# Kernel tuning notes

Measured on AMD Instinct MI355X. Metric: run time of the kernel, lower is better.

Reference implementation:

```python
import jax, jax.numpy as jnp
import numpy as np

EPS = 1e-8

def _cosine_rows(a, b):
    na = jnp.maximum(jnp.linalg.norm(a, axis=1), EPS)
    nb = jnp.maximum(jnp.linalg.norm(b, axis=1), EPS)
    return jnp.sum(a * b, axis=1) / (na * nb)


def setup_inputs() -> dict:
    key = jax.random.key(0)
    k1, k2 = jax.random.split(key)
    X = jax.random.normal(k1, (16384, 1024), dtype=jnp.float32)
    dictionary = jax.random.normal(k2, (4096, 1024), dtype=jnp.float32)
    descriptors = jnp.arange(4096, dtype=jnp.int64)
    return {"X": X, "dictionary": dictionary, "descriptors": descriptors, "k": 16}


def reference(X, dictionary, descriptors, k):
    # SOMP with centering=True, criterion='l1', pc=None (default forward path)
    orig_X = X
    std_orig_sum = jnp.sum(jnp.var(orig_X, axis=0, ddof=1))
    X_mean = jnp.mean(X, axis=0, keepdims=True)   # [1, D]
    Xc = X - X_mean                               # centered data [N, D]

    M = dictionary.shape[0]
    notchosen = jnp.ones((M,), dtype=X.dtype)
    residual = Xc
    chosen, evr, l2, cosine = [], [], [], []
    W = None
    recon = jnp.zeros_like(Xc)

    for i in range(k):  # k is a static Python int -> unrolled, per-step shapes static
        cross = residual @ dictionary.T           # [N, M] -- dominant memory traffic
        scores = jnp.sum(jnp.abs(cross * notchosen), axis=0)  # l1 criterion
        idx = jnp.argmax(scores)
        chosen.append(idx)
        notchosen = notchosen.at[idx].set(0)

        atoms = dictionary[jnp.stack(chosen)]     # [i+1, D], dynamic gather, static shape
        # least squares: min ||atoms.T @ W - Xc.T||  (full column rank -> normal eqs)
        G = atoms @ atoms.T                       # [i+1, i+1]
        W = jnp.linalg.solve(G, atoms @ Xc.T)     # [i+1, N]
        recon = (atoms.T @ W).T                   # [N, D]
        residual = Xc - recon

        rec_full = X_mean + recon
        evr.append(jnp.sum(jnp.var(rec_full, axis=0, ddof=1)) / std_orig_sum)
        cosine.append(jnp.mean(_cosine_rows(orig_X, rec_full)))
        l2.append(jnp.mean((orig_X - rec_full) ** 2))

    weights = jnp.linalg.norm(W, axis=1)          # [k]
    chosen_arr = jnp.stack(chosen)
    recon_out = X_mean + recon
    residual_out = Xc - recon                     # == X - recon_out
    return (recon_out, residual_out, chosen_arr, weights, W.T,
            jnp.stack(evr), jnp.stack(l2), jnp.stack(cosine))
```

## Files before the change

### kernel.cpp

```cpp
#include <hip/hip_runtime.h>
#include <math.h>

#define NROWS 16384
#define DIMK  1024
#define MDIC  4096
#define KSEL  16

#define OFF_RECON   0
#define OFF_RESID   ((size_t)NROWS*DIMK)
#define OFF_CHOSEN  ((size_t)2*NROWS*DIMK)
#define OFF_WEIGHTS (OFF_CHOSEN + 16)
#define OFF_WT      (OFF_WEIGHTS + 16)
#define OFF_EVR     (OFF_WT + (size_t)NROWS*KSEL)
#define OFF_L2      (OFF_EVR + 16)
#define OFF_COS     (OFF_L2 + 16)

typedef unsigned short u16;
typedef unsigned long long u64;
typedef __attribute__((ext_vector_type(8))) short short8;
typedef __attribute__((ext_vector_type(4))) float f32x4;

__device__ inline float blockReduce256f(float v) {
    __shared__ float ws_[4];
    #pragma unroll
    for (int off = 32; off > 0; off >>= 1) v += __shfl_down(v, off);
    __syncthreads();
    if ((threadIdx.x & 63) == 0) ws_[threadIdx.x >> 6] = v;
    __syncthreads();
    return ws_[0] + ws_[1] + ws_[2] + ws_[3];
}

__device__ inline void wredStore(double v, int k, int lane, int wv, double (*accS)[4]) {
    #pragma unroll
    for (int off = 32; off > 0; off >>= 1) v += __shfl_down(v, off);
    if (lane == 0) accS[k][wv] = v;
}

__device__ inline u16 f2bf(float f) {
    unsigned u = __float_as_uint(f);
    unsigned r = u + 0x7FFFu + ((u >> 16) & 1u);
    return (u16)(r >> 16);
}
__device__ inline float bf2f(u16 h) { return __uint_as_float(((unsigned)h) << 16); }

__global__ void k_init(float* notchosen, u64* amx, u64* statsAcc, u64* ctr2) {
    int m = blockIdx.x * 256 + threadIdx.x;
    if (m < MDIC) notchosen[m] = 1.0f;
    if (blockIdx.x == 0) {
        if (threadIdx.x < 40) statsAcc[threadIdx.x] = 0ULL;
        if (threadIdx.x < 2)  amx[threadIdx.x] = 0ULL;
        if (threadIdx.x == 0) *ctr2 = 0ULL;
    }
}

__global__ __launch_bounds__(256) void k_colstats(const float* __restrict__ X,
                                                  float* __restrict__ colpart,
                                                  float* __restrict__ sqpart) {
    int d  = blockIdx.x * 256 + threadIdx.x;
    int r0 = blockIdx.y * 256;
    float s = 0.f, sq = 0.f;
    for (int r = 0; r < 256; ++r) {
        float v = X[(size_t)(r0 + r) * DIMK + d];
        s += v; sq += v * v;
    }
    colpart[(size_t)blockIdx.y * DIMK + d] = s;
    __shared__ float red[256];
    red[threadIdx.x] = sq; __syncthreads();
    for (int off = 128; off > 0; off >>= 1) {
        if (threadIdx.x < off) red[threadIdx.x] += red[threadIdx.x + off];
        __syncthreads();
    }
    if (threadIdx.x == 0) sqpart[blockIdx.y * 4 + blockIdx.x] = red[0];
}

__global__ __launch_bounds__(1024) void k_reduce_mean(const float* __restrict__ colpart,
                                                      const float* __restrict__ sqpart,
                                                      float* __restrict__ xmean,
                                                      double* __restrict__ scal) {
    int d = threadIdx.x;
    double s = 0.0;
    for (int y = 0; y < 64; ++y) s += (double)colpart[(size_t)y * DIMK + d];
    float m = (float)(s / (double)NROWS);
    xmean[d] = m;
    __shared__ double red[1024];
    red[d] = (double)m * (double)m; __syncthreads();
    for (int off = 512; off > 0; off >>= 1) {
        if (d < off) red[d] += red[d + off];
        __syncthreads();
    }
    if (d == 0) {
        double xmn2 = red[0];
        double sx2 = 0.0;
        for (int i = 0; i < 256; ++i) sx2 += (double)sqpart[i];
        scal[0] = sx2;
        scal[1] = sx2 - (double)NROWS * xmn2;
        scal[2] = xmn2;
    }
}

__global__ __launch_bounds__(256) void k_md(const float* __restrict__ Dict,
                                            const float* __restrict__ xmean,
                                            float* __restrict__ md,
                                            float* __restrict__ Dnorm2) {
    int m = blockIdx.x, t = threadIdx.x;
    float4 a = ((const float4*)(Dict + (size_t)m * DIMK))[t];
    float4 b = ((const float4*)xmean)[t];
    float s  = a.x * b.x + a.y * b.y + a.z * b.z + a.w * b.w;
    float sn = a.x * a.x + a.y * a.y + a.z * a.z + a.w * a.w;
    s  = blockReduce256f(s);
    sn = blockReduce256f(sn);
    if (t == 0) { md[m] = s; Dnorm2[m] = sn; }
}

__global__ __launch_bounds__(256) void k_split(const float* __restrict__ src,
                                               u16* __restrict__ hi,
                                               u16* __restrict__ lo) {
    size_t idx = ((size_t)blockIdx.x * 256 + threadIdx.x) * 4;
    float4 v = *(const float4*)(src + idx);
    ushort4 h, l;
    h.x = f2bf(v.x); l.x = f2bf(v.x - bf2f(h.x));
    h.y = f2bf(v.y); l.y = f2bf(v.y - bf2f(h.y));
    h.z = f2bf(v.z); l.z = f2bf(v.z - bf2f(h.z));
    h.w = f2bf(v.w); l.w = f2bf(v.w - bf2f(h.w));
    *(ushort4*)(hi + idx) = h;
    *(ushort4*)(lo + idx) = l;
}

__global__ __launch_bounds__(256) void k_splitX(const float* __restrict__ src,
                                                u16* __restrict__ hi,
                                                u16* __restrict__ lo,
                                                const float* __restrict__ xmean,
                                                float* __restrict__ Xnorm2,
                                                float* __restrict__ XdotM) {
    int n = blockIdx.x, t = threadIdx.x;
    size_t idx = (size_t)n * DIMK + t * 4;
    float4 v = *(const float4*)(src + idx);
    float4 mv = ((const float4*)xmean)[t];
    ushort4 h, l;
    h.x = f2bf(v.x); l.x = f2bf(v.x - bf2f(h.x));
    h.y = f2bf(v.y); l.y = f2bf(v.y - bf2f(h.y));
    h.z = f2bf(v.z); l.z = f2bf(v.z - bf2f(h.z));
    h.w = f2bf(v.w); l.w = f2bf(v.w - bf2f(h.w));
    *(ushort4*)(hi + idx) = h;
    *(ushort4*)(lo + idx) = l;
    float s2 = v.x * v.x + v.y * v.y + v.z * v.z + v.w * v.w;
    float sm = v.x * mv.x + v.y * mv.y + v.z * mv.z + v.w * mv.w;
    s2 = blockReduce256f(s2);
    sm = blockReduce256f(sm);
    if (t == 0) { Xnorm2[n] = s2; XdotM[n] = sm; }
}

__global__ __launch_bounds__(256) void k_gemm_mfma(const u16* __restrict__ Ahi,
                                                   const u16* __restrict__ Alo,
                                                   const u16* __restrict__ Bhi,
                                                   const u16* __restrict__ Blo,
                                                   const float* __restrict__ md,
                                                   u16* __restrict__ C0h,
                                                   int rowAbase) {
    __shared__ u16 sAh[128 * 32];
    __shared__ u16 sAl[128 * 32];
    __shared__ u16 sBh[128 * 32];
    __shared__ u16 sBl[128 * 32];
    int tid  = threadIdx.x;
    int wave = tid >> 6, lane = tid & 63;
    int rowA0 = blockIdx.y * 128;
    int rowB0 = blockIdx.x * 128;

    const u16* gsrc = (wave == 0) ? Ahi : (wave == 1) ? Alo : (wave == 2) ? Bhi : Blo;
    u16* sdst       = (wave == 0) ? sAh : (wave == 1) ? sAl : (wave == 2) ? sBh : sBl;
    int grow0 = (wave < 2) ? rowA0 : rowB0;
    const u16* gbase = gsrc + (size_t)(grow0 + (lane >> 2)) * DIMK + ((lane & 3) << 3);

    f32x4 zero = {0.f, 0.f, 0.f, 0.f};
    f32x4 acc[4][4];
    #pragma unroll
    for (int i = 0; i < 4; ++i)
        #pragma unroll
        for (int j = 0; j < 4; ++j) acc[i][j] = zero;

    int lm = lane & 15, lk = lane >> 4;
    int wi = wave >> 1, wj = wave & 1;

    for (int k0 = 0; k0 < DIMK; k0 += 32) {
        __syncthreads();
        #pragma unroll
        for (int i = 0; i < 8; ++i) {
            __builtin_amdgcn_global_load_lds(
                (__attribute__((address_space(1))) void*)(gbase + k0 + (size_t)i * 16 * DIMK),
                (__attribute__((address_space(3))) void*)(sdst + i * 512),
                16, 0, 0);
        }
        __syncthreads();
        short8 ah[4], al[4], bh[4], bl[4];
        #pragma unroll
        for (int f = 0; f < 4; ++f) {
            int ra = (wi * 64 + f * 16 + lm) * 32 + lk * 8;
            ah[f] = *(const short8*)&sAh[ra];
            al[f] = *(const short8*)&sAl[ra];
            int rb = (wj * 64 + f * 16 + lm) * 32 + lk * 8;
            bh[f] = *(const short8*)&sBh[rb];
            bl[f] = *(const short8*)&sBl[rb];
        }
        #pragma unroll
        for (int fi = 0; fi < 4; ++fi)
            #pragma unroll
            for (int fj = 0; fj < 4; ++fj) {
                acc[fi][fj] = __builtin_amdgcn_mfma_f32_16x16x32_bf16(ah[fi], bh[fj], acc[fi][fj], 0, 0, 0);
                acc[fi][fj] = __builtin_amdgcn_mfma_f32_16x16x32_bf16(ah[fi], bl[fj], acc[fi][fj], 0, 0, 0);
                acc[fi][fj] = __builtin_amdgcn_mfma_f32_16x16x32_bf16(al[fi], bh[fj], acc[fi][fj], 0, 0, 0);
            }
    }
    #pragma unroll
    for (int fj = 0; fj < 4; ++fj) {
        int m = rowB0 + wj * 64 + fj * 16 + lm;
        float mdv = md[m];
        #pragma unroll
        for (int fi = 0; fi < 4; ++fi) {
            int nb = rowAbase + rowA0 + wi * 64 + fi * 16 + lk * 4;
            #pragma unroll
            for (int r = 0; r < 4; ++r)
                C0h[(size_t)(nb + r) * MDIC + m] = f2bf(acc[fi][fj][r] - mdv);
        }
    }
}

template <int NA>
__global__ __launch_bounds__(256) void k_score(const u16* __restrict__ C0h,
                                               const float* __restrict__ GR,
                                               const float* __restrict__ Wm,
                                               float* __restrict__ scorePf) {
    constexpr int NAX = NA ? NA : 1;
    __shared__ float Wl[NAX][64];
    int t = threadIdx.x;
    int m0 = blockIdx.x * 1024 + t * 4;
    int n0 = blockIdx.y * 64;
    float4 gr[NAX];
    #pragma unroll
    for (int j = 0; j < NA; ++j) gr[j] = *(const float4*)&GR[(size_t)j * MDIC + m0];
    for (int idx = t; idx < NA * 64; idx += 256) {
        int j = idx >> 6, nn = idx & 63;
        Wl[j][nn] = Wm[(size_t)j * NROWS + n0 + nn];
    }
    __syncthreads();
    float4 acc = {0.f, 0.f, 0.f, 0.f};
    for (int nn = 0; nn < 64; ++nn) {
        ushort4 ch = *(const ushort4*)&C0h[(size_t)(n0 + nn) * MDIC + m0];
        float4 c = {bf2f(ch.x), bf2f(ch.y), bf2f(ch.z), bf2f(ch.w)};
        float4 cr = {0.f, 0.f, 0.f, 0.f};
        #pragma unroll
        for (int j = 0; j < NA; ++j) {
            float wv = Wl[j][nn];
            cr.x += wv * gr[j].x; cr.y += wv * gr[j].y;
            cr.z += wv * gr[j].z; cr.w += wv * gr[j].w;
        }
        acc.x += fabsf(c.x - cr.x); acc.y += fabsf(c.y - cr.y);
        acc.z += fabsf(c.z - cr.z); acc.w += fabsf(c.w - cr.w);
    }
    *(float4*)&scorePf[(size_t)blockIdx.y * MDIC + m0] = acc;
}

__global__ __launch_bounds__(256) void k_scoreargmax(const float* __restrict__ scorePf,
                                                     float* __restrict__ notchosen,
                                                     u64* __restrict__ amx,
                                                     int* __restrict__ chosen,
                                                     float* __restrict__ outChosen,
                                                     const float* __restrict__ md,
                                                     const float* __restrict__ Dnorm2,
                                                     const float* __restrict__ GR,
                                                     float* __restrict__ Lmat,
                                                     float* __restrict__ Gcc,
                                                     float* __restrict__ mdot,
                                                     int iter) {
    int t = threadIdx.x;
    int m0 = blockIdx.x * 256;
    int tm = t & 63, yg = t >> 6;
    float sx = 0.f, sy = 0.f, sz = 0.f, sw = 0.f;
    #pragma unroll 4
    for (int y = yg; y < 256; y += 4) {
        float4 v = *(const float4*)&scorePf[(size_t)y * MDIC + m0 + (tm << 2)];
        sx += v.x; sy += v.y; sz += v.z; sw += v.w;
    }
    __shared__ float4 red4[4][64];
    float4 pv; pv.x = sx; pv.y = sy; pv.z = sz; pv.w = sw;
    red4[yg][tm] = pv;
    __syncthreads();
    u64 best = 0ULL;
    if (t < 64) {
        float4 a = red4[0][t], b = red4[1][t], cc = red4[2][t], d = red4[3][t];
        double sv[4] = {(double)a.x + b.x + cc.x + d.x,
                        (double)a.y + b.y + cc.y + d.y,
                        (double)a.z + b.z + cc.z + d.z,
                        (double)a.w + b.w + cc.w + d.w};
        int mb = m0 + (t << 2);
        #pragma unroll
        for (int j = 0; j < 4; ++j) {
            if (notchosen[mb + j] != 0.f) {
                u64 key = ((u64)__double_as_longlong(sv[j]) & ~0xFFFULL) | (u64)(4095 - (mb + j));
                if (key > best) best = key;
            }
        }
        #pragma unroll
        for (int off = 32; off > 0; off >>= 1) {
            u64 o = __shfl_down(best, off);
            if (o > best) best = o;
        }
    }
    __shared__ int slast, sc;
    if (t == 0) {
        atomicMax(&amx[0], best);
        __threadfence();
        u64 done = atomicAdd(&amx[1], 1ULL);
        slast = (done == 15ULL) ? 1 : 0;
        if (slast) {
            u64 k = atomicMax(&amx[0], 0ULL);
            int c = 4095 - (int)(k & 0xFFFULL);
            sc = c;
            chosen[iter] = c;
            notchosen[c] = 0.f;
            outChosen[iter] = (float)c;
            mdot[iter] = md[c];
            amx[0] = 0ULL; amx[1] = 0ULL;
        }
    }
    __syncthreads();
    if (!slast) return;
    int c = sc;
    __shared__ float Lsh[16][16];
    __shared__ float g[17];
    __shared__ float LrowS[16];
    Lsh[t >> 4][t & 15] = Lmat[t];
    if (t < iter)  g[t] = GR[(size_t)t * MDIC + c];
    if (t == iter) g[t] = Dnorm2[c];
    __syncthreads();
    if (t == 0) {
        for (int b = 0; b < iter; ++b) {
            float s = g[b];
            for (int x = 0; x < b; ++x) s -= LrowS[x] * Lsh[b][x];
            LrowS[b] = s / Lsh[b][b];
        }
        float s2 = g[iter];
        for (int x = 0; x < iter; ++x) s2 -= LrowS[x] * LrowS[x];
        LrowS[iter] = sqrtf(fmaxf(s2, 1e-20f));
        for (int b = 0; b <= iter; ++b) Lmat[iter * 16 + b] = LrowS[b];
        for (int b = iter + 1; b < 16; ++b) Lmat[iter * 16 + b] = 0.f;
        for (int b = 0; b < iter; ++b) { Gcc[iter * 16 + b] = g[b]; Gcc[b * 16 + iter] = g[b]; }
        Gcc[iter * 16 + iter] = g[iter];
    }
}

template <int NAT>
__global__ __launch_bounds__(256) void k_gramsolve(const float* __restrict__ Dict,
                                                   const int* __restrict__ chosen,
                                                   const u16* __restrict__ C0h,
                                                   float* __restrict__ GR,
                                                   float* __restrict__ Bm,
                                                   const float* __restrict__ Lmat,
                                                   const float* __restrict__ Gcc_g,
                                                   const float* __restrict__ mdot,
                                                   const float* __restrict__ Xnorm2,
                                                   const float* __restrict__ XdotM,
                                                   const double* __restrict__ scal,
                                                   float* __restrict__ Wm,
                                                   u64* __restrict__ statsAcc,
                                                   u64* __restrict__ ctr2,
                                                   float* __restrict__ out, int iter) {
    int t = threadIdx.x;
    int c = chosen[iter];
    if (blockIdx.x >= 64) {
        int m = blockIdx.x - 64;
        float4 a = ((const float4*)(Dict + (size_t)c * DIMK))[t];
        float4 b = ((const float4*)(Dict + (size_t)m * DIMK))[t];
        float s = a.x * b.x + a.y * b.y + a.z * b.z + a.w * b.w;
        s = blockReduce256f(s);
        if (t == 0) GR[(size_t)iter * MDIC + m] = s;
        return;
    }
    constexpr int NV = 3 + 2 * NAT;
    __shared__ float L[16][16];
    __shared__ float G[16][16];
    __shared__ float mdl[16];
    __shared__ double accS[35][4];
    if (t < NAT * NAT) {
        int a = t / NAT, b2 = t % NAT;
        L[a][b2] = Lmat[a * 16 + b2];
        G[a][b2] = Gcc_g[a * 16 + b2];
    }
    if (t < NAT) mdl[t] = mdot[t];
    __syncthreads();
    int n = blockIdx.x * 256 + t;
    float b[NAT], y[NAT], w[NAT];
    #pragma unroll
    for (int j = 0; j < NAT - 1; ++j) b[j] = Bm[(size_t)j * NROWS + n];
    float bn = bf2f(C0h[(size_t)n * MDIC + c]);
    b[NAT - 1] = bn;
    Bm[(size_t)(NAT - 1) * NROWS + n] = bn;
    #pragma unroll
    for (int a = 0; a < NAT; ++a) {
        float s = b[a];
        #pragma unroll
        for (int x = 0; x < NAT; ++x) if (x < a) s -= L[a][x] * y[x];
        y[a] = s / L[a][a];
    }
    #pragma unroll
    for (int a = NAT - 1; a >= 0; --a) {
        float s = y[a];
        #pragma unroll
        for (int x = 0; x < NAT; ++x) if (x > a) s -= L[x][a] * w[x];
        w[a] = s / L[a][a];
    }
    #pragma unroll
    for (int j = 0; j < NAT; ++j) Wm[(size_t)j * NROWS + n] = w[j];

    float q = 0.f, wb = 0.f, wmd = 0.f, num1 = 0.f;
    #pragma unroll
    for (int j = 0; j < NAT; ++j) {
        float gw = 0.f;
        #pragma unroll
        for (int x = 0; x < NAT; ++x) gw += G[j][x] * w[x];
        q    += w[j] * gw;
        wb   += w[j] * b[j];
        wmd  += w[j] * mdl[j];
        num1 += w[j] * (b[j] + mdl[j]);
    }
    float xmn2 = (float)scal[2];
    float rec2 = xmn2 + 2.f * wmd + q;
    float na = fmaxf(sqrtf(Xnorm2[n]), 1e-8f);
    float nb = fmaxf(sqrtf(fmaxf(rec2, 0.f)), 1e-8f);
    float cosn = (XdotM[n] + num1) / (na * nb);

    int lane = t & 63, wv = t >> 6;
    wredStore((double)q,    0, lane, wv, accS);
    wredStore((double)wb,   1, lane, wv, accS);
    wredStore((double)cosn, 2, lane, wv, accS);
    #pragma unroll
    for (int j = 0; j < NAT; ++j) {
        wredStore((double)w[j],                 3 + j,       lane, wv, accS);
        wredStore((double)w[j] * (double)w[j],  3 + NAT + j, lane, wv, accS);
    }
    __syncthreads();
    if (t < NV) {
        double tot = accS[t][0] + accS[t][1] + accS[t][2] + accS[t][3];
        long long fx = (long long)(tot * 1048576.0);
        atomicAdd(&statsAcc[t], (u64)fx);
    }
    __shared__ int slast2;
    __syncthreads();
    if (t == 0) {
        __threadfence();
        slast2 = (atomicAdd(ctr2, 1ULL) == 63ULL) ? 1 : 0;
    }
    __syncthreads();
    if (!slast2) return;
    __shared__ double stot[35];
    __shared__ double wbarS[16];
    if (t < NV) {
        u64 raw = atomicAdd(&statsAcc[t], 0ULL);
        stot[t] = (double)(long long)raw * (1.0 / 1048576.0);
        statsAcc[t] = 0ULL;
    }
    if (t == 0) *ctr2 = 0ULL;
    __syncthreads();
    if (t < NAT) wbarS[t] = stot[3 + t] * (1.0 / (double)NROWS);
    __syncthreads();
    if (t == 0) {
        double q2 = stot[0], wb2 = stot[1], cs = stot[2];
        double wg = 0.0;
        for (int a = 0; a < NAT; ++a)
            for (int b2 = 0; b2 < NAT; ++b2) wg += wbarS[a] * wbarS[b2] * (double)G[a][b2];
        double sumXc2 = scal[1];
        out[OFF_EVR + iter] = (float)((q2 - (double)NROWS * wg) / sumXc2);
        out[OFF_L2  + iter] = (float)((sumXc2 - 2.0 * wb2 + q2) / ((double)NROWS * (double)DIMK));
        out[OFF_COS + iter] = (float)(cs / (double)NROWS);
        if (NAT == KSEL) {
            for (int j = 0; j < NAT; ++j)
                out[OFF_WEIGHTS + j] = (float)sqrt(stot[3 + NAT + j]);
        }
    }
}

__global__ __launch_bounds__(256) void k_outfinal(const float* __restrict__ X,
                                                  const float* __restrict__ xmean,
                                                  const float* __restrict__ Dict,
                                                  const int* __restrict__ chosen,
                                                  const float* __restrict__ Wm,
                                                  float* __restrict__ out) {
    __shared__ int cI[16];
    int t = threadIdx.x;
    if (t < 16) cI[t] = chosen[t];
    __syncthreads();
    int n0 = blockIdx.x * 8;
    if (t < 128) {
        int j = t & 15, r = t >> 4;
        int n = n0 + r;
        out[OFF_WT + (size_t)n * 16 + j] = Wm[(size_t)j * NROWS + n];
    }
    float4 xm = ((const float4*)xmean)[t];
    for (int r = 0; r < 8; ++r) {
        int n = n0 + r;
        float w[16];
        #pragma unroll
        for (int j = 0; j < 16; ++j) w[j] = Wm[(size_t)j * NROWS + n];
        float4 rec = xm;
        #pragma unroll
        for (int j = 0; j < 16; ++j) {
            float4 a = ((const float4*)(Dict + (size_t)cI[j] * DIMK))[t];
            rec.x += w[j] * a.x; rec.y += w[j] * a.y;
            rec.z += w[j] * a.z; rec.w += w[j] * a.w;
        }
        float4 xv = ((const float4*)(X + (size_t)n * DIMK))[t];
        float4 res = {xv.x - rec.x, xv.y - rec.y, xv.z - rec.z, xv.w - rec.w};
        ((float4*)(out + OFF_RECON + (size_t)n * DIMK))[t] = rec;
        ((float4*)(out + OFF_RESID + (size_t)n * DIMK))[t] = res;
    }
}

struct IterArgs {
    const float *X, *Dict;
    u16 *C0h;
    float *GR, *W, *Bm, *md, *Dnorm2, *xmean, *Xnorm2, *XdotM, *notchosen, *Lmat, *Gcc, *mdot;
    float *scorePf;
    u64 *amx, *statsAcc, *ctr2;
    double *scal;
    int *chosen;
    float *out;
    hipStream_t stream;
};

template <int I>
static void run_iter(const IterArgs& a) {
    k_score<I><<<dim3(4, 256), 256, 0, a.stream>>>(a.C0h, a.GR, a.W, a.scorePf);
    k_scoreargmax<<<16, 256, 0, a.stream>>>(a.scorePf, a.notchosen, a.amx, a.chosen,
                                            a.out + OFF_CHOSEN, a.md, a.Dnorm2, a.GR,
                                            a.Lmat, a.Gcc, a.mdot, I);
    k_gramsolve<I + 1><<<MDIC + 64, 256, 0, a.stream>>>(a.Dict, a.chosen, a.C0h, a.GR,
                                                        a.Bm, a.Lmat, a.Gcc, a.mdot,
                                                        a.Xnorm2, a.XdotM, a.scal, a.W,
                                                        a.statsAcc, a.ctr2, a.out, I);
}

template <int I>
struct Loop {
    static void go(const IterArgs& a) { run_iter<I>(a); Loop<I + 1>::go(a); }
};
template <>
struct Loop<KSEL> { static void go(const IterArgs&) {} };

extern "C" void kernel_launch(void* const* d_in, const int* in_sizes, int n_in,
                              void* d_out, int out_size, void* d_ws, size_t ws_size,
                              hipStream_t stream) {
    (void)in_sizes; (void)n_in; (void)out_size;
    const float* X    = (const float*)d_in[0];
    const float* Dict = (const float*)d_in[1];
    float* out = (float*)d_out;

    char* ws = (char*)d_ws;
    size_t off = 0;
    auto carve = [&](size_t bytes) -> char* {
        char* p = ws + off;
        off += (bytes + 255) & ~(size_t)255;
        return p;
    };
    u16*    C0h       = (u16*)   carve((size_t)NROWS * MDIC * 2);
    float*  GR        = (float*) carve((size_t)KSEL * MDIC * 4);
    float*  W         = (float*) carve((size_t)KSEL * NROWS * 4);
    float*  Bm        = (float*) carve((size_t)KSEL * NROWS * 4);
    float*  md        = (float*) carve((size_t)MDIC * 4);
    float*  Dnorm2    = (float*) carve((size_t)MDIC * 4);
    float*  xmean     = (float*) carve((size_t)DIMK * 4);
    float*  colpart   = (float*) carve((size_t)64 * DIMK * 4);
    float*  sqpart    = (float*) carve(256 * 4);
    float*  Xnorm2    = (float*) carve((size_t)NROWS * 4);
    float*  XdotM     = (float*) carve((size_t)NROWS * 4);
    float*  scorePf   = (float*) carve((size_t)256 * MDIC * 4);
    float*  notchosen = (float*) carve((size_t)MDIC * 4);
    u64*    amx       = (u64*)   carve(2 * 8);
    u64*    statsAcc  = (u64*)   carve(40 * 8);
    u64*    ctr2      = (u64*)   carve(8);
    int*    chosen    = (int*)   carve(KSEL * 4);
    float*  Lmat      = (float*) carve(256 * 4);
    float*  Gcc       = (float*) carve(256 * 4);
    float*  mdot      = (float*) carve(16 * 4);
    double* scal      = (double*)carve(8 * 8);
    u16*    Bhi       = (u16*)   carve((size_t)MDIC * DIMK * 2);
    u16*    Blo       = (u16*)   carve((size_t)MDIC * DIMK * 2);

    int chunkrows = 0;
    for (int cr = NROWS; cr >= 128; cr >>= 1) {
        size_t need = (size_t)cr * DIMK * 2 * 2 + 512;
        if (off + need <= ws_size) { chunkrows = cr; break; }
    }
    if (chunkrows == 0) chunkrows = 128;
    u16* Ahi = (u16*) carve((size_t)chunkrows * DIMK * 2);
    u16* Alo = (u16*) carve((size_t)chunkrows * DIMK * 2);

    k_init<<<MDIC / 256, 256, 0, stream>>>(notchosen, amx, statsAcc, ctr2);
    k_colstats<<<dim3(4, 64), 256, 0, stream>>>(X, colpart, sqpart);
    k_reduce_mean<<<1, 1024, 0, stream>>>(colpart, sqpart, xmean, scal);
    k_md<<<MDIC, 256, 0, stream>>>(Dict, xmean, md, Dnorm2);

    k_split<<<(MDIC * DIMK) / 1024, 256, 0, stream>>>(Dict, Bhi, Blo);
    int nchunks = NROWS / chunkrows;
    for (int c = 0; c < nchunks; ++c) {
        k_splitX<<<chunkrows, 256, 0, stream>>>(
            X + (size_t)c * chunkrows * DIMK, Ahi, Alo, xmean,
            Xnorm2 + (size_t)c * chunkrows, XdotM + (size_t)c * chunkrows);
        k_gemm_mfma<<<dim3(MDIC / 128, chunkrows / 128), 256, 0, stream>>>(
            Ahi, Alo, Bhi, Blo, md, C0h, c * chunkrows);
    }

    IterArgs a{X, Dict, C0h, GR, W, Bm, md, Dnorm2, xmean, Xnorm2, XdotM, notchosen,
               Lmat, Gcc, mdot, scorePf, amx, statsAcc, ctr2, scal, chosen, out, stream};
    Loop<0>::go(a);

    k_outfinal<<<NROWS / 8, 256, 0, stream>>>(X, xmean, Dict, chosen, W, out);
}
```

Baseline: 1.471 ms.

## Replace split-bf16 GEMM with 256x256 double-buffered 8-wave pipelined MFMA kernel

Rewrites the initial cross-product GEMM as a 256x256 tile kernel with 8 waves, double-buffered LDS and XOR-swizzled layout. The three bf16 hi/lo products are folded into one extended K loop of 3072 (hi*hi, lo*hi, hi*lo segments), with async global-to-LDS loads interleaved into four compute phases per step. It also adds XCD-aware block remapping and setprio around the MFMA issue. The goal is higher MFMA utilisation and better overlap of loads with compute. The risks are register pressure from the 8x4 accumulator tile and correctness of the hand-written vmcnt waits.

```diff
diff --git a/kernel.cpp b/kernel.cpp
--- a/kernel.cpp
+++ b/kernel.cpp
@@ -150,76 +150,134 @@
     if (t == 0) { Xnorm2[n] = s2; XdotM[n] = sm; }
 }
 
-__global__ __launch_bounds__(256) void k_gemm_mfma(const u16* __restrict__ Ahi,
-                                                   const u16* __restrict__ Alo,
-                                                   const u16* __restrict__ Bhi,
-                                                   const u16* __restrict__ Blo,
-                                                   const float* __restrict__ md,
-                                                   u16* __restrict__ C0h,
-                                                   int rowAbase) {
-    __shared__ u16 sAh[128 * 32];
-    __shared__ u16 sAl[128 * 32];
-    __shared__ u16 sBh[128 * 32];
-    __shared__ u16 sBl[128 * 32];
-    int tid  = threadIdx.x;
-    int wave = tid >> 6, lane = tid & 63;
-    int rowA0 = blockIdx.y * 128;
-    int rowB0 = blockIdx.x * 128;
-
-    const u16* gsrc = (wave == 0) ? Ahi : (wave == 1) ? Alo : (wave == 2) ? Bhi : Blo;
-    u16* sdst       = (wave == 0) ? sAh : (wave == 1) ? sAl : (wave == 2) ? sBh : sBl;
-    int grow0 = (wave < 2) ? rowA0 : rowB0;
-    const u16* gbase = gsrc + (size_t)(grow0 + (lane >> 2)) * DIMK + ((lane & 3) << 3);
-
+
+#define GLL16(g, l) __builtin_amdgcn_global_load_lds( \
+    (__attribute__((address_space(1))) void*)(g), \
+    (__attribute__((address_space(3))) void*)(l), 16, 0, 0)
+
+#define STAGE_A2(pa_, kc_, wb_, q0_, q1_) do { \
+    GLL16((pa_) + aGbase + (size_t)(q0_) * 64 * DIMK + (kc_), \
+          sA + (wb_) * 16384 + (q0_) * 4096 + lWbase); \
+    GLL16((pa_) + aGbase + (size_t)(q1_) * 64 * DIMK + (kc_), \
+          sA + (wb_) * 16384 + (q1_) * 4096 + lWbase); \
+} while (0)
+
+#define STAGE_B2(pb_, kc_, wb_, q0_, q1_) do { \
+    GLL16((pb_) + bGbase + (size_t)(q0_) * 64 * DIMK + (kc_), \
+          sB + (wb_) * 16384 + (q0_) * 4096 + lWbase); \
+    GLL16((pb_) + bGbase + (size_t)(q1_) * 64 * DIMK + (kc_), \
+          sB + (wb_) * 16384 + (q1_) * 4096 + lWbase); \
+} while (0)
+
+#define VM4 asm volatile("s_waitcnt vmcnt(4)" ::: "memory")
+#define VM2 asm volatile("s_waitcnt vmcnt(2)" ::: "memory")
+#define VM0 asm volatile("s_waitcnt vmcnt(0)" ::: "memory")
+#define NOPSTMT ((void)0)
+
+#define PHASE(rb_, mq_, nq_, STAGE_STMT, WAIT_STMT) do { \
+    short8 af[4][2], bfv[2][2]; \
+    const u16* pA_ = sA + (rb_) * 16384; \
+    const u16* pB_ = sB + (rb_) * 16384; \
+    _Pragma("unroll") \
+    for (int fi = 0; fi < 4; ++fi) { \
+        af[fi][0] = *(const short8*)&pA_[aoffA0 + ((mq_) * 4 + fi) * 1024]; \
+        af[fi][1] = *(const short8*)&pA_[aoffA1 + ((mq_) * 4 + fi) * 1024]; \
+    } \
+    _Pragma("unroll") \
+    for (int fj = 0; fj < 2; ++fj) { \
+        bfv[fj][0] = *(const short8*)&pB_[boffB0 + ((nq_) * 2 + fj) * 1024]; \
+        bfv[fj][1] = *(const short8*)&pB_[boffB1 + ((nq_) * 2 + fj) * 1024]; \
+    } \
+    STAGE_STMT; \
+    __builtin_amdgcn_s_barrier(); \
+    __builtin_amdgcn_s_setprio(1); \
+    _Pragma("unroll") \
+    for (int fi = 0; fi < 4; ++fi) \
+        _Pragma("unroll") \
+        for (int fj = 0; fj < 2; ++fj) { \
+            acc[(mq_) * 4 + fi][(nq_) * 2 + fj] = __builtin_amdgcn_mfma_f32_16x16x32_bf16( \
+                af[fi][0], bfv[fj][0], acc[(mq_) * 4 + fi][(nq_) * 2 + fj], 0, 0, 0); \
+            acc[(mq_) * 4 + fi][(nq_) * 2 + fj] = __builtin_amdgcn_mfma_f32_16x16x32_bf16( \
+                af[fi][1], bfv[fj][1], acc[(mq_) * 4 + fi][(nq_) * 2 + fj], 0, 0, 0); \
+        } \
+    __builtin_amdgcn_s_setprio(0); \
+    WAIT_STMT; \
+    __builtin_amdgcn_s_barrier(); \
+} while (0)
+
+__global__ __launch_bounds__(512, 2) void k_gemm8(const u16* __restrict__ Ahi,
+                                                  const u16* __restrict__ Alo,
+                                                  const u16* __restrict__ Bhi,
+                                                  const u16* __restrict__ Blo,
+                                                  const float* __restrict__ md,
+                                                  u16* __restrict__ C0h,
+                                                  int rowAbase) {
+    __shared__ u16 sA[2 * 16384];
+    __shared__ u16 sB[2 * 16384];
+    int T = threadIdx.x;
+    int lane = T & 63, wid = T >> 6;
+    int wr = wid >> 2, wc = wid & 3;
+
+    int nwg = gridDim.x, cpx = nwg >> 3;
+    int bid = blockIdx.x;
+    int wg  = (bid & 7) * cpx + (bid >> 3);
+    int bm = wg >> 4, bn = wg & 15;
+    int rowA0 = bm * 256, rowB0 = bn * 256;
+
+    int sw = (T & 7) ^ ((T >> 3) & 7);
+    size_t aGbase = (size_t)(rowA0 + (T >> 3)) * DIMK + sw * 8;
+    size_t bGbase = (size_t)(rowB0 + (T >> 3)) * DIMK + sw * 8;
+    int lWbase = (T >> 6) * 512;
+
+    int lm = lane & 15, lk = lane >> 4;
+    int kb0 = (lk * 16) ^ ((lane & 7) << 4);
+    int kb1 = (64 + lk * 16) ^ ((lane & 7) << 4);
+    int aoffA0 = (wr * 128 + lm) * 64 + (kb0 >> 1);
+    int aoffA1 = (wr * 128 + lm) * 64 + (kb1 >> 1);
+    int boffB0 = (wc * 64 + lm) * 64 + (kb0 >> 1);
+    int boffB1 = (wc * 64 + lm) * 64 + (kb1 >> 1);
+
+    f32x4 acc[8][4];
     f32x4 zero = {0.f, 0.f, 0.f, 0.f};
-    f32x4 acc[4][4];
-    #pragma unroll
-    for (int i = 0; i < 4; ++i)
+    #pragma unroll
+    for (int i = 0; i < 8; ++i)
         #pragma unroll
         for (int j = 0; j < 4; ++j) acc[i][j] = zero;
 
-    int lm = lane & 15, lk = lane >> 4;
-    int wi = wave >> 1, wj = wave & 1;
-
-    for (int k0 = 0; k0 < DIMK; k0 += 32) {
-        __syncthreads();
-        #pragma unroll
-        for (int i = 0; i < 8; ++i) {
-            __builtin_amdgcn_global_load_lds(
-                (__attribute__((address_space(1))) void*)(gbase + k0 + (size_t)i * 16 * DIMK),
-                (__attribute__((address_space(3))) void*)(sdst + i * 512),
-                16, 0, 0);
-        }
-        __syncthreads();
-        short8 ah[4], al[4], bh[4], bl[4];
-        #pragma unroll
-        for (int f = 0; f < 4; ++f) {
-            int ra = (wi * 64 + f * 16 + lm) * 32 + lk * 8;
-            ah[f] = *(const short8*)&sAh[ra];
-            al[f] = *(const short8*)&sAl[ra];
-            int rb = (wj * 64 + f * 16 + lm) * 32 + lk * 8;
-            bh[f] = *(const short8*)&sBh[rb];
-            bl[f] = *(const short8*)&sBl[rb];
-        }
-        #pragma unroll
-        for (int fi = 0; fi < 4; ++fi)
-            #pragma unroll
-            for (int fj = 0; fj < 4; ++fj) {
-                acc[fi][fj] = __builtin_amdgcn_mfma_f32_16x16x32_bf16(ah[fi], bh[fj], acc[fi][fj], 0, 0, 0);
-                acc[fi][fj] = __builtin_amdgcn_mfma_f32_16x16x32_bf16(ah[fi], bl[fj], acc[fi][fj], 0, 0, 0);
-                acc[fi][fj] = __builtin_amdgcn_mfma_f32_16x16x32_bf16(al[fi], bh[fj], acc[fi][fj], 0, 0, 0);
-            }
-    }
-    #pragma unroll
-    for (int fj = 0; fj < 4; ++fj) {
-        int m = rowB0 + wj * 64 + fj * 16 + lm;
+    STAGE_B2(Bhi, 0, 0, 0, 1);
+    STAGE_B2(Bhi, 0, 0, 2, 3);
+    STAGE_A2(Ahi, 0, 0, 0, 2);
+    STAGE_A2(Ahi, 0, 0, 1, 3);
+    VM2;
+    __builtin_amdgcn_s_barrier();
+
+    for (int t = 0; t < 47; ++t) {
+        int rbuf = t & 1, wbuf = rbuf ^ 1;
+        int kk = (t + 1) << 6;
+        int seg = kk >> 10;
+        const u16* pa = (seg == 1) ? Alo : Ahi;
+        const u16* pb = (seg == 2) ? Blo : Bhi;
+        int kc = kk & 1023;
+        PHASE(rbuf, 0, 0, STAGE_B2(pb, kc, wbuf, 0, 1), NOPSTMT);
+        PHASE(rbuf, 0, 1, STAGE_B2(pb, kc, wbuf, 2, 3), VM4);
+        PHASE(rbuf, 1, 0, STAGE_A2(pa, kc, wbuf, 0, 2), NOPSTMT);
+        PHASE(rbuf, 1, 1, STAGE_A2(pa, kc, wbuf, 1, 3), VM2);
+    }
+    PHASE(1, 0, 0, NOPSTMT, NOPSTMT);
+    PHASE(1, 0, 1, NOPSTMT, VM0);
+    PHASE(1, 1, 0, NOPSTMT, NOPSTMT);
+    PHASE(1, 1, 1, NOPSTMT, NOPSTMT);
+
+    #pragma unroll
+    for (int nf = 0; nf < 4; ++nf) {
+        int m = rowB0 + wc * 64 + nf * 16 + lm;
         float mdv = md[m];
         #pragma unroll
-        for (int fi = 0; fi < 4; ++fi) {
-            int nb = rowAbase + rowA0 + wi * 64 + fi * 16 + lk * 4;
+        for (int mf = 0; mf < 8; ++mf) {
+            int nb = rowAbase + rowA0 + wr * 128 + mf * 16 + lk * 4;
             #pragma unroll
             for (int r = 0; r < 4; ++r)
-                C0h[(size_t)(nb + r) * MDIC + m] = f2bf(acc[fi][fj][r] - mdv);
+                C0h[(size_t)(nb + r) * MDIC + m] = f2bf(acc[mf][nf][r] - mdv);
         }
     }
 }
@@ -585,11 +643,11 @@
     u16*    Blo       = (u16*)   carve((size_t)MDIC * DIMK * 2);
 
     int chunkrows = 0;
-    for (int cr = NROWS; cr >= 128; cr >>= 1) {
+    for (int cr = NROWS; cr >= 256; cr >>= 1) {
         size_t need = (size_t)cr * DIMK * 2 * 2 + 512;
         if (off + need <= ws_size) { chunkrows = cr; break; }
     }
-    if (chunkrows == 0) chunkrows = 128;
+    if (chunkrows == 0) chunkrows = 256;
     u16* Ahi = (u16*) carve((size_t)chunkrows * DIMK * 2);
     u16* Alo = (u16*) carve((size_t)chunkrows * DIMK * 2);
 
@@ -604,7 +662,8 @@
         k_splitX<<<chunkrows, 256, 0, stream>>>(
             X + (size_t)c * chunkrows * DIMK, Ahi, Alo, xmean,
             Xnorm2 + (size_t)c * chunkrows, XdotM + (size_t)c * chunkrows);
-        k_gemm_mfma<<<dim3(MDIC / 128, chunkrows / 128), 256, 0, stream>>>(
+        int mtiles = chunkrows / 256;
+        k_gemm8<<<dim3(mtiles * 16), 512, 0, stream>>>(
             Ahi, Alo, Bhi, Blo, md, C0h, c * chunkrows);
     }
 
```

After: 1.524 ms. +3.6%, slower.
